# Kernel optimization log

Hardware: AMD Instinct MI355X
Metric: run time of the kernel (lower is better)

Reference implementation:

```python
import jax, jax.numpy as jnp
import numpy as np

MARGIN = 0.3


def setup_inputs() -> dict:
    key = jax.random.key(0)
    k1, k2 = jax.random.split(key)
    inputs = jax.random.normal(k1, (8192, 256), dtype=jnp.float32)
    targets = jax.random.randint(k2, (8192,), 0, 512, dtype=jnp.int64)
    return {"inputs": inputs, "targets": targets}


def reference(inputs, targets):
    # L2-normalize features (normalize_feature=True default)
    x = inputs / (jnp.linalg.norm(inputs, axis=-1, keepdims=True) + 1e-12)
    n = x.shape[0]
    # pairwise euclidean distance [n, n]
    sq = jnp.sum(x * x, axis=1)
    dist = sq[:, None] + sq[None, :] - 2.0 * (x @ x.T)
    dist = jnp.sqrt(jnp.clip(dist, 1e-12, None))
    # positive / negative masks
    same = targets[:, None] == targets[None, :]
    eye = jnp.eye(n, dtype=bool)
    is_same = same & ~eye          # positives, diagonal excluded
    is_diff = ~same                # negatives
    neg_inf = jnp.float32(-jnp.inf)
    pos_inf = jnp.float32(jnp.inf)
    # hard positive: max over positives per row (fallback 0.0 if none)
    dist_ap = jnp.max(jnp.where(is_same, dist, neg_inf), axis=1)
    dist_ap = jnp.where(jnp.any(is_same, axis=1), dist_ap, 0.0)
    # hard negative: min over negatives per row (fallback margin+1 if none)
    dist_an = jnp.min(jnp.where(is_diff, dist, pos_inf), axis=1)
    dist_an = jnp.where(jnp.any(is_diff, axis=1), dist_an, MARGIN + 1.0)
    # MarginRankingLoss with y=1: mean(max(0, -(an - ap) + margin))
    loss = jnp.mean(jnp.maximum(0.0, dist_ap - dist_an + MARGIN))
    return loss
```

## Files before the change

### kernel.cpp

```cpp
#include <hip/hip_runtime.h>
#include <hip/hip_bf16.h>

#define NROWS  8192
#define DIM    256
#define NCLASS 512
#define MARGIN 0.3f

using bf16x8 = __attribute__((ext_vector_type(8))) short;
using f32x4  = __attribute__((ext_vector_type(4))) float;

__device__ inline ushort f2bf(float f) {
    __hip_bfloat16 h = __float2bfloat16(f);
    return *reinterpret_cast<ushort*>(&h);
}
__device__ inline float bf2f(ushort u) {
    return __uint_as_float(((unsigned)u) << 16);
}
__device__ inline unsigned f2ord(float f) {
    unsigned b = __float_as_uint(f);
    return (b & 0x80000000u) ? ~b : (b | 0x80000000u);
}
__device__ inline float ord2f(unsigned u) {
    return __uint_as_float((u & 0x80000000u) ? (u & 0x7FFFFFFFu) : ~u);
}
__device__ inline void ld16_g2l(const void* g, void* l) {
    __builtin_amdgcn_global_load_lds(
        (const __attribute__((address_space(1))) unsigned int*)g,
        (__attribute__((address_space(3))) unsigned int*)l, 16, 0, 0);
}

#define XBS_OFF 0u
#define SQS_OFF 4194304u
#define TGT_OFF 4227072u
#define PMX_OFF 4259840u
#define NMN_OFF 4292608u
#define BIN_OFF 4325376u
#define ACC_OFF 4327424u
#define TIK_OFF 4327432u

__global__ __launch_bounds__(512) void hist_scan_kernel(
    const int* __restrict__ tgt, int* __restrict__ bincur,
    double* __restrict__ accd, unsigned* __restrict__ ticket)
{
    __shared__ int h[NCLASS];
    int tid = threadIdx.x;
    h[tid] = 0;
    if (tid == 0) { *accd = 0.0; *ticket = 0u; }
    __syncthreads();
    for (int k = 0; k < NROWS / NCLASS; ++k)
        atomicAdd(&h[tgt[tid + k * NCLASS]], 1);
    __syncthreads();
    int cnt = h[tid];
    for (int ofs = 1; ofs < NCLASS; ofs <<= 1) {
        int v = (tid >= ofs) ? h[tid - ofs] : 0;
        __syncthreads();
        h[tid] += v;
        __syncthreads();
    }
    bincur[tid] = h[tid] - cnt;
}

__global__ __launch_bounds__(256) void norm_scatter_kernel(
    const float* __restrict__ in, const int* __restrict__ tgt,
    int* __restrict__ bincur, ushort* __restrict__ xbs,
    float* __restrict__ sqs, int* __restrict__ tgts,
    unsigned* __restrict__ pmax, unsigned* __restrict__ nmin)
{
    int row  = blockIdx.x * 4 + (threadIdx.x >> 6);
    int lane = threadIdx.x & 63;
    float4 v = ((const float4*)(in + (size_t)row * DIM))[lane];
    float ss = v.x * v.x + v.y * v.y + v.z * v.z + v.w * v.w;
#pragma unroll
    for (int m = 1; m < 64; m <<= 1) ss += __shfl_xor(ss, m, 64);
    float inv = 1.0f / (sqrtf(ss) + 1e-12f);

    ushort4 st;
    st.x = f2bf(v.x * inv); st.y = f2bf(v.y * inv);
    st.z = f2bf(v.z * inv); st.w = f2bf(v.w * inv);

    int t = 0, dst = 0;
    if (lane == 0) { t = tgt[row]; dst = atomicAdd(&bincur[t], 1); }
    dst = __shfl(dst, 0); t = __shfl(t, 0);

    ((ushort4*)(xbs + (size_t)dst * DIM))[lane] = st;

    float a0 = bf2f(st.x), a1 = bf2f(st.y), a2 = bf2f(st.z), a3 = bf2f(st.w);
    float s2 = a0 * a0 + a1 * a1 + a2 * a2 + a3 * a3;
#pragma unroll
    for (int m = 1; m < 64; m <<= 1) s2 += __shfl_xor(s2, m, 64);
    if (lane == 0) {
        sqs[dst]  = s2;
        tgts[dst] = t;
        pmax[dst] = 0x007FFFFFu;
        nmin[dst] = 0xFF800000u;
    }
}

__global__ __launch_bounds__(256, 2) void gram_kernel(
    const ushort* __restrict__ xbs, const float* __restrict__ sqs,
    const int* __restrict__ tgts, unsigned* __restrict__ pmax,
    unsigned* __restrict__ nmin)
{
    __shared__ struct {
        char  buf[2][16384];
        float sqc[512];
        int   tgc[512];
        int   tga[256];
    } sm;

    const int wave = threadIdx.x >> 6;
    const int lane = threadIdx.x & 63;
    const int l15  = lane & 15;
    const int quad = lane >> 4;
    const int mbase = blockIdx.x * 256 + wave * 64;
    const int nbase = blockIdx.y * 512;

    {
        int c = threadIdx.x * 2;
        sm.sqc[c]     = sqs[nbase + c];
        sm.sqc[c + 1] = sqs[nbase + c + 1];
        sm.tgc[c]     = tgts[nbase + c];
        sm.tgc[c + 1] = tgts[nbase + c + 1];
        sm.tga[threadIdx.x] = tgts[blockIdx.x * 256 + threadIdx.x];
    }

    bf16x8 afrag[4][8];
#pragma unroll
    for (int a = 0; a < 4; ++a) {
        const ushort* arow = xbs + (size_t)(mbase + a * 16 + l15) * DIM + quad * 8;
#pragma unroll
        for (int kk = 0; kk < 8; ++kk)
            afrag[a][kk] = *(const bf16x8*)(arow + kk * 32);
    }
    const int rlo = tgts[mbase];
    const int rhi = tgts[mbase + 63];

    const int colh = lane >> 5, c31 = lane & 31;
    int offs[4];
#pragma unroll
    for (int j = 0; j < 4; ++j)
        offs[j] = colh * 512 + ((c31 ^ ((2 * j + colh) & 7)) << 4);

    const char* xbs_b = (const char*)xbs;

    {
        const char* gbase = xbs_b + (size_t)nbase * 512;
#pragma unroll
        for (int j = 0; j < 4; ++j) {
            int i = wave * 4 + j;
            ld16_g2l(gbase + i * 1024 + offs[j], sm.buf[0] + i * 1024);
        }
    }
    __syncthreads();

    float pm[16], nm[16];
#pragma unroll
    for (int j = 0; j < 16; ++j) { pm[j] = -__builtin_inff(); nm[j] = __builtin_inff(); }

#pragma unroll 2
    for (int s = 0; s < 16; ++s) {
        if (s < 15) {
            const char* gbase = xbs_b + (size_t)(nbase + (s + 1) * 32) * 512;
            char* lbase = sm.buf[(s + 1) & 1];
#pragma unroll
            for (int j = 0; j < 4; ++j) {
                int i = wave * 4 + j;
                ld16_g2l(gbase + i * 1024 + offs[j], lbase + i * 1024);
            }
        }
        const char* bufc = sm.buf[s & 1];
#pragma unroll
        for (int u = 0; u < 2; ++u) {
            const int t16 = s * 32 + u * 16;
            bf16x8 bfrag[8];
#pragma unroll
            for (int kk = 0; kk < 8; ++kk)
                bfrag[kk] = *(const bf16x8*)(bufc + u * 8192 + l15 * 512 +
                                             (((quad + 4 * kk) ^ (l15 & 7)) << 4));
            f32x4 acc4[4];
#pragma unroll
            for (int a = 0; a < 4; ++a) {
                f32x4 acc = {0.f, 0.f, 0.f, 0.f};
#pragma unroll
                for (int kk = 0; kk < 8; ++kk)
                    acc = __builtin_amdgcn_mfma_f32_16x16x32_bf16(afrag[a][kk], bfrag[kk], acc, 0, 0, 0);
                acc4[a] = acc;
            }
            const float sqc = sm.sqc[t16 + l15];
            const int clo = sm.tgc[t16], chi = sm.tgc[t16 + 15];
            if (rlo <= chi && clo <= rhi) {
                const int tc = sm.tgc[t16 + l15];
#pragma unroll
                for (int a = 0; a < 4; ++a)
#pragma unroll
                    for (int i = 0; i < 4; ++i) {
                        const float v = fmaf(acc4[a][i], -2.0f, sqc);
                        const bool same = (sm.tga[wave * 64 + a * 16 + quad * 4 + i] == tc);
                        pm[a * 4 + i] = fmaxf(pm[a * 4 + i], same ? v : -__builtin_inff());
                        nm[a * 4 + i] = fminf(nm[a * 4 + i], same ? __builtin_inff() : v);
                    }
            } else {
#pragma unroll
                for (int a = 0; a < 4; ++a)
#pragma unroll
                    for (int i = 0; i < 4; ++i)
                        nm[a * 4 + i] = fminf(nm[a * 4 + i], fmaf(acc4[a][i], -2.0f, sqc));
            }
        }
        __syncthreads();
    }

#pragma unroll
    for (int m = 1; m < 16; m <<= 1) {
#pragma unroll
        for (int j = 0; j < 16; ++j) {
            pm[j] = fmaxf(pm[j], __shfl_xor(pm[j], m, 64));
            nm[j] = fminf(nm[j], __shfl_xor(nm[j], m, 64));
        }
    }
    if (l15 == 0) {
#pragma unroll
        for (int a = 0; a < 4; ++a)
#pragma unroll
            for (int i = 0; i < 4; ++i) {
                int r = mbase + a * 16 + quad * 4 + i;
                atomicMax(&pmax[r], f2ord(pm[a * 4 + i]));
                atomicMin(&nmin[r], f2ord(nm[a * 4 + i]));
            }
    }
}

__global__ __launch_bounds__(256) void finalize_kernel(
    const unsigned* __restrict__ pmax, const unsigned* __restrict__ nmin,
    const float* __restrict__ sqs, double* __restrict__ accd,
    unsigned* __restrict__ ticket, float* __restrict__ out)
{
    int r = blockIdx.x * 256 + threadIdx.x;
    float pe = ord2f(pmax[r]);
    float ne = ord2f(nmin[r]);
    float ap = sqrtf(fmaxf(sqs[r] + pe, 0.0f));
    float an = (ne > 1e30f) ? (MARGIN + 1.0f) : sqrtf(fmaxf(sqs[r] + ne, 0.0f));
    float h  = fmaxf(ap - an + MARGIN, 0.0f);
    double s = (double)h;
#pragma unroll
    for (int m = 1; m < 64; m <<= 1) s += __shfl_xor(s, m, 64);
    __shared__ double sh[4];
    if ((threadIdx.x & 63) == 0) sh[threadIdx.x >> 6] = s;
    __syncthreads();
    if (threadIdx.x == 0) {
        double b = sh[0] + sh[1] + sh[2] + sh[3];
        atomicAdd(accd, b);
        __threadfence();
        unsigned old = atomicAdd(ticket, 1u);
        if (old == gridDim.x - 1) {
            double total = atomicAdd(accd, 0.0);
            out[0] = (float)(total / (double)NROWS);
        }
    }
}

extern "C" void kernel_launch(void* const* d_in, const int* in_sizes, int n_in,
                              void* d_out, int out_size, void* d_ws, size_t ws_size,
                              hipStream_t stream) {
    const float* in  = (const float*)d_in[0];
    const int*   tgt = (const int*)d_in[1];
    float*       out = (float*)d_out;

    char* ws = (char*)d_ws;
    ushort*   xbs    = (ushort*)(ws + XBS_OFF);
    float*    sqs    = (float*)(ws + SQS_OFF);
    int*      tgts   = (int*)(ws + TGT_OFF);
    unsigned* pmax   = (unsigned*)(ws + PMX_OFF);
    unsigned* nmin   = (unsigned*)(ws + NMN_OFF);
    int*      bincur = (int*)(ws + BIN_OFF);
    double*   accd   = (double*)(ws + ACC_OFF);
    unsigned* ticket = (unsigned*)(ws + TIK_OFF);

    hist_scan_kernel<<<1, 512, 0, stream>>>(tgt, bincur, accd, ticket);
    norm_scatter_kernel<<<NROWS / 4, 256, 0, stream>>>(in, tgt, bincur, xbs, sqs, tgts, pmax, nmin);
    gram_kernel<<<dim3(32, 16), 256, 0, stream>>>(xbs, sqs, tgts, pmax, nmin);
    finalize_kernel<<<32, 256, 0, stream>>>(pmax, nmin, sqs, accd, ticket, out);
}
```

Measured before the change: 113.9 us.

## Fuse all stages into one persistent kernel with grid barriers and permutation indirection

Replaces the four launches (histogram/scan, normalize+scatter, gram, finalize) with a single 512-block kernel that uses software grid barriers between phases and a last-block ticket for the final reduction. Rows are no longer physically scattered into class order; instead block 0 builds a permutation, and the gram phase gathers rows through it. The intent is to remove launch gaps and the extra scatter writes. In exchange it adds a serial single-block phase (scan plus an 8192-row perm build), spin-wait barriers that assume all 512 blocks are co-resident, indirect gathered loads, and a memset launch.

```diff
diff --git a/kernel.cpp b/kernel.cpp
--- a/kernel.cpp
+++ b/kernel.cpp
@@ -4,7 +4,11 @@
 #define NROWS  8192
 #define DIM    256
 #define NCLASS 512
+#define NBLK   512
 #define MARGIN 0.3f
+
+#define ORD_NEGINF 0x007FFFFFu
+#define ORD_POSINF 0xFF800000u
 
 using bf16x8 = __attribute__((ext_vector_type(8))) short;
 using f32x4  = __attribute__((ext_vector_type(4))) float;
@@ -29,126 +33,146 @@
         (__attribute__((address_space(3))) unsigned int*)l, 16, 0, 0);
 }
 
-#define XBS_OFF 0u
-#define SQS_OFF 4194304u
-#define TGT_OFF 4227072u
-#define PMX_OFF 4259840u
-#define NMN_OFF 4292608u
-#define BIN_OFF 4325376u
-#define ACC_OFF 4327424u
-#define TIK_OFF 4327432u
-
-__global__ __launch_bounds__(512) void hist_scan_kernel(
-    const int* __restrict__ tgt, int* __restrict__ bincur,
-    double* __restrict__ accd, unsigned* __restrict__ ticket)
+#define XB_OFF   0u
+#define SQU_OFF  4194304u
+#define PRM_OFF  4227072u
+#define SQS_OFF  4259840u
+#define TGS_OFF  4292608u
+#define PMX_OFF  4325376u
+#define NMN_OFF  4358144u
+#define META_OFF 4390912u
+
+struct SM {
+    char  buf[2][16384];
+    float sqc[512];
+    int   tgc[512];
+    int   prm[512];
+    int   tga[256];
+};
+
+__device__ inline void grid_barrier(unsigned* cnt) {
+    __syncthreads();
+    if (threadIdx.x == 0) {
+        __threadfence();
+        atomicAdd(cnt, 1u);
+        while (atomicAdd(cnt, 0u) < NBLK) __builtin_amdgcn_s_sleep(2);
+        __threadfence();
+    }
+    __syncthreads();
+}
+
+__global__ __launch_bounds__(256, 2) void fused_kernel(
+    const float* __restrict__ in, const int* __restrict__ tgt,
+    ushort* __restrict__ xb, float* __restrict__ squ,
+    int* __restrict__ perm, float* __restrict__ sqs, int* __restrict__ tgts,
+    unsigned* __restrict__ pmax, unsigned* __restrict__ nmin,
+    int* __restrict__ bins, unsigned* __restrict__ bar1,
+    unsigned* __restrict__ bar2, unsigned* __restrict__ ticket,
+    float* __restrict__ out)
 {
-    __shared__ int h[NCLASS];
-    int tid = threadIdx.x;
-    h[tid] = 0;
-    if (tid == 0) { *accd = 0.0; *ticket = 0u; }
-    __syncthreads();
-    for (int k = 0; k < NROWS / NCLASS; ++k)
-        atomicAdd(&h[tgt[tid + k * NCLASS]], 1);
-    __syncthreads();
-    int cnt = h[tid];
-    for (int ofs = 1; ofs < NCLASS; ofs <<= 1) {
-        int v = (tid >= ofs) ? h[tid - ofs] : 0;
-        __syncthreads();
-        h[tid] += v;
-        __syncthreads();
-    }
-    bincur[tid] = h[tid] - cnt;
-}
-
-__global__ __launch_bounds__(256) void norm_scatter_kernel(
-    const float* __restrict__ in, const int* __restrict__ tgt,
-    int* __restrict__ bincur, ushort* __restrict__ xbs,
-    float* __restrict__ sqs, int* __restrict__ tgts,
-    unsigned* __restrict__ pmax, unsigned* __restrict__ nmin)
-{
-    int row  = blockIdx.x * 4 + (threadIdx.x >> 6);
-    int lane = threadIdx.x & 63;
-    float4 v = ((const float4*)(in + (size_t)row * DIM))[lane];
-    float ss = v.x * v.x + v.y * v.y + v.z * v.z + v.w * v.w;
-#pragma unroll
-    for (int m = 1; m < 64; m <<= 1) ss += __shfl_xor(ss, m, 64);
-    float inv = 1.0f / (sqrtf(ss) + 1e-12f);
-
-    ushort4 st;
-    st.x = f2bf(v.x * inv); st.y = f2bf(v.y * inv);
-    st.z = f2bf(v.z * inv); st.w = f2bf(v.w * inv);
-
-    int t = 0, dst = 0;
-    if (lane == 0) { t = tgt[row]; dst = atomicAdd(&bincur[t], 1); }
-    dst = __shfl(dst, 0); t = __shfl(t, 0);
-
-    ((ushort4*)(xbs + (size_t)dst * DIM))[lane] = st;
-
-    float a0 = bf2f(st.x), a1 = bf2f(st.y), a2 = bf2f(st.z), a3 = bf2f(st.w);
-    float s2 = a0 * a0 + a1 * a1 + a2 * a2 + a3 * a3;
-#pragma unroll
-    for (int m = 1; m < 64; m <<= 1) s2 += __shfl_xor(s2, m, 64);
-    if (lane == 0) {
-        sqs[dst]  = s2;
-        tgts[dst] = t;
-        pmax[dst] = 0x007FFFFFu;
-        nmin[dst] = 0xFF800000u;
-    }
-}
-
-__global__ __launch_bounds__(256, 2) void gram_kernel(
-    const ushort* __restrict__ xbs, const float* __restrict__ sqs,
-    const int* __restrict__ tgts, unsigned* __restrict__ pmax,
-    unsigned* __restrict__ nmin)
-{
-    __shared__ struct {
-        char  buf[2][16384];
-        float sqc[512];
-        int   tgc[512];
-        int   tga[256];
-    } sm;
-
-    const int wave = threadIdx.x >> 6;
-    const int lane = threadIdx.x & 63;
+    __shared__ SM sm;
+    __shared__ unsigned lastflag;
+    const int b    = blockIdx.x;
+    const int tid  = threadIdx.x;
+    const int wave = tid >> 6;
+    const int lane = tid & 63;
     const int l15  = lane & 15;
     const int quad = lane >> 4;
-    const int mbase = blockIdx.x * 256 + wave * 64;
-    const int nbase = blockIdx.y * 512;
+
+#pragma unroll
+    for (int i = 0; i < 4; ++i) {
+        int row = b * 16 + wave * 4 + i;
+        float4 v = ((const float4*)(in + (size_t)row * DIM))[lane];
+        float ss = v.x * v.x + v.y * v.y + v.z * v.z + v.w * v.w;
+#pragma unroll
+        for (int m = 1; m < 64; m <<= 1) ss += __shfl_xor(ss, m, 64);
+        float inv = 1.0f / (sqrtf(ss) + 1e-12f);
+        ushort4 st;
+        st.x = f2bf(v.x * inv); st.y = f2bf(v.y * inv);
+        st.z = f2bf(v.z * inv); st.w = f2bf(v.w * inv);
+        ((ushort4*)(xb + (size_t)row * DIM))[lane] = st;
+        float a0 = bf2f(st.x), a1 = bf2f(st.y), a2 = bf2f(st.z), a3 = bf2f(st.w);
+        float s2 = a0 * a0 + a1 * a1 + a2 * a2 + a3 * a3;
+#pragma unroll
+        for (int m = 1; m < 64; m <<= 1) s2 += __shfl_xor(s2, m, 64);
+        if (lane == 0) {
+            squ[row]  = s2;
+            pmax[row] = ORD_NEGINF;
+            nmin[row] = ORD_POSINF;
+            atomicAdd(&bins[tgt[row]], 1);
+        }
+    }
+    grid_barrier(bar1);
+
+    if (b == 0) {
+        int* sc  = (int*)sm.buf[0];
+        int* cur = sc + NCLASS;
+        const int c0 = tid, c1 = tid + 256;
+        sc[c0] = atomicAdd(&bins[c0], 0);
+        sc[c1] = atomicAdd(&bins[c1], 0);
+        __syncthreads();
+        int n0 = sc[c0], n1 = sc[c1];
+        for (int ofs = 1; ofs < NCLASS; ofs <<= 1) {
+            int v0 = (c0 >= ofs) ? sc[c0 - ofs] : 0;
+            int v1 = (c1 >= ofs) ? sc[c1 - ofs] : 0;
+            __syncthreads();
+            sc[c0] += v0; sc[c1] += v1;
+            __syncthreads();
+        }
+        cur[c0] = sc[c0] - n0;
+        cur[c1] = sc[c1] - n1;
+        __syncthreads();
+        for (int it = 0; it < NROWS / 256; ++it) {
+            int r = it * 256 + tid;
+            int c = tgt[r];
+            int slot = atomicAdd(&cur[c], 1);
+            perm[slot] = r;
+            sqs[slot]  = squ[r];
+            tgts[slot] = c;
+        }
+    }
+    grid_barrier(bar2);
+
+    const int bx = b >> 4;
+    const int by = b & 15;
+    const int mbase = bx * 256 + wave * 64;
+    const int nbase = by * 512;
 
     {
-        int c = threadIdx.x * 2;
+        int c = tid * 2;
         sm.sqc[c]     = sqs[nbase + c];
         sm.sqc[c + 1] = sqs[nbase + c + 1];
         sm.tgc[c]     = tgts[nbase + c];
         sm.tgc[c + 1] = tgts[nbase + c + 1];
-        sm.tga[threadIdx.x] = tgts[blockIdx.x * 256 + threadIdx.x];
-    }
+        sm.prm[c]     = perm[nbase + c];
+        sm.prm[c + 1] = perm[nbase + c + 1];
+        sm.tga[tid]   = tgts[bx * 256 + tid];
+    }
+    __syncthreads();
 
     bf16x8 afrag[4][8];
 #pragma unroll
     for (int a = 0; a < 4; ++a) {
-        const ushort* arow = xbs + (size_t)(mbase + a * 16 + l15) * DIM + quad * 8;
+        int grow = perm[mbase + a * 16 + l15];
+        const ushort* arow = xb + (size_t)grow * DIM + quad * 8;
 #pragma unroll
         for (int kk = 0; kk < 8; ++kk)
             afrag[a][kk] = *(const bf16x8*)(arow + kk * 32);
     }
-    const int rlo = tgts[mbase];
-    const int rhi = tgts[mbase + 63];
+    const int rlo = sm.tga[wave * 64];
+    const int rhi = sm.tga[wave * 64 + 63];
 
     const int colh = lane >> 5, c31 = lane & 31;
-    int offs[4];
-#pragma unroll
-    for (int j = 0; j < 4; ++j)
-        offs[j] = colh * 512 + ((c31 ^ ((2 * j + colh) & 7)) << 4);
-
-    const char* xbs_b = (const char*)xbs;
+    const char* xb_b = (const char*)xb;
 
     {
-        const char* gbase = xbs_b + (size_t)nbase * 512;
 #pragma unroll
         for (int j = 0; j < 4; ++j) {
             int i = wave * 4 + j;
-            ld16_g2l(gbase + i * 1024 + offs[j], sm.buf[0] + i * 1024);
+            int col = 2 * i + colh;
+            int prow = sm.prm[col];
+            ld16_g2l(xb_b + (size_t)prow * 512 + ((c31 ^ (col & 7)) << 4),
+                     sm.buf[0] + i * 1024);
         }
     }
     __syncthreads();
@@ -160,12 +184,14 @@
 #pragma unroll 2
     for (int s = 0; s < 16; ++s) {
         if (s < 15) {
-            const char* gbase = xbs_b + (size_t)(nbase + (s + 1) * 32) * 512;
             char* lbase = sm.buf[(s + 1) & 1];
 #pragma unroll
             for (int j = 0; j < 4; ++j) {
                 int i = wave * 4 + j;
-                ld16_g2l(gbase + i * 1024 + offs[j], lbase + i * 1024);
+                int col = 2 * i + colh;
+                int prow = sm.prm[(s + 1) * 32 + col];
+                ld16_g2l(xb_b + (size_t)prow * 512 + ((c31 ^ (col & 7)) << 4),
+                         lbase + i * 1024);
             }
         }
         const char* bufc = sm.buf[s & 1];
@@ -228,34 +254,31 @@
                 atomicMin(&nmin[r], f2ord(nm[a * 4 + i]));
             }
     }
-}
-
-__global__ __launch_bounds__(256) void finalize_kernel(
-    const unsigned* __restrict__ pmax, const unsigned* __restrict__ nmin,
-    const float* __restrict__ sqs, double* __restrict__ accd,
-    unsigned* __restrict__ ticket, float* __restrict__ out)
-{
-    int r = blockIdx.x * 256 + threadIdx.x;
-    float pe = ord2f(pmax[r]);
-    float ne = ord2f(nmin[r]);
-    float ap = sqrtf(fmaxf(sqs[r] + pe, 0.0f));
-    float an = (ne > 1e30f) ? (MARGIN + 1.0f) : sqrtf(fmaxf(sqs[r] + ne, 0.0f));
-    float h  = fmaxf(ap - an + MARGIN, 0.0f);
-    double s = (double)h;
-#pragma unroll
-    for (int m = 1; m < 64; m <<= 1) s += __shfl_xor(s, m, 64);
-    __shared__ double sh[4];
-    if ((threadIdx.x & 63) == 0) sh[threadIdx.x >> 6] = s;
-    __syncthreads();
-    if (threadIdx.x == 0) {
-        double b = sh[0] + sh[1] + sh[2] + sh[3];
-        atomicAdd(accd, b);
+
+    __syncthreads();
+    if (tid == 0) {
         __threadfence();
-        unsigned old = atomicAdd(ticket, 1u);
-        if (old == gridDim.x - 1) {
-            double total = atomicAdd(accd, 0.0);
-            out[0] = (float)(total / (double)NROWS);
-        }
+        unsigned arrived = atomicAdd(ticket, 1u) + 1;
+        lastflag = (arrived == NBLK) ? 1u : 0u;
+    }
+    __syncthreads();
+    if (lastflag) {
+        double s = 0.0;
+        for (int it = 0; it < NROWS / 256; ++it) {
+            int r = it * 256 + tid;
+            float pe = ord2f(atomicMax(&pmax[r], ORD_NEGINF));
+            float ne = ord2f(atomicMin(&nmin[r], ORD_POSINF));
+            float ap = sqrtf(fmaxf(sqs[r] + pe, 0.0f));
+            float an = (ne > 1e30f) ? (MARGIN + 1.0f) : sqrtf(fmaxf(sqs[r] + ne, 0.0f));
+            float h  = fmaxf(ap - an + MARGIN, 0.0f);
+            s += (double)h;
+        }
+#pragma unroll
+        for (int m = 1; m < 64; m <<= 1) s += __shfl_xor(s, m, 64);
+        double* shd = (double*)sm.buf[0];
+        if (lane == 0) shd[wave] = s;
+        __syncthreads();
+        if (tid == 0) out[0] = (float)((shd[0] + shd[1] + shd[2] + shd[3]) / (double)NROWS);
     }
 }
 
@@ -267,17 +290,19 @@
     float*       out = (float*)d_out;
 
     char* ws = (char*)d_ws;
-    ushort*   xbs    = (ushort*)(ws + XBS_OFF);
+    ushort*   xb     = (ushort*)(ws + XB_OFF);
+    float*    squ    = (float*)(ws + SQU_OFF);
+    int*      perm   = (int*)(ws + PRM_OFF);
     float*    sqs    = (float*)(ws + SQS_OFF);
-    int*      tgts   = (int*)(ws + TGT_OFF);
+    int*      tgts   = (int*)(ws + TGS_OFF);
     unsigned* pmax   = (unsigned*)(ws + PMX_OFF);
     unsigned* nmin   = (unsigned*)(ws + NMN_OFF);
-    int*      bincur = (int*)(ws + BIN_OFF);
-    double*   accd   = (double*)(ws + ACC_OFF);
-    unsigned* ticket = (unsigned*)(ws + TIK_OFF);
-
-    hist_scan_kernel<<<1, 512, 0, stream>>>(tgt, bincur, accd, ticket);
-    norm_scatter_kernel<<<NROWS / 4, 256, 0, stream>>>(in, tgt, bincur, xbs, sqs, tgts, pmax, nmin);
-    gram_kernel<<<dim3(32, 16), 256, 0, stream>>>(xbs, sqs, tgts, pmax, nmin);
-    finalize_kernel<<<32, 256, 0, stream>>>(pmax, nmin, sqs, accd, ticket, out);
-}
+    int*      bins   = (int*)(ws + META_OFF);
+    unsigned* bar1   = (unsigned*)(ws + META_OFF + 2048);
+    unsigned* bar2   = (unsigned*)(ws + META_OFF + 2052);
+    unsigned* ticket = (unsigned*)(ws + META_OFF + 2056);
+
+    hipMemsetAsync(ws + META_OFF, 0, 4096, stream);
+    fused_kernel<<<NBLK, 256, 0, stream>>>(in, tgt, xb, squ, perm, sqs, tgts,
+                                           pmax, nmin, bins, bar1, bar2, ticket, out);
+}
```

Result: slower. 217.9 us (+91.3%).

## Store B tiles in fragment-major LDS layout with 64-column stages

Applied to the files above, without the earlier changes.

Reorganizes the LDS staging of B (column) rows so each wave loads 16 rows directly into an MFMA-fragment-ordered layout, so each lane reads contiguous 16-byte chunks at lane*16 with no XOR swizzle. Stage size doubles from 32 to 64 columns (LDS buffers grow to 2x32KB) and the stage count halves, reducing barriers and prefetch overhead. The larger shared memory footprint may reduce occupancy under launch_bounds(256,2). The global loads now read 64-byte strided pieces per row, which may coalesce less well.

```diff
diff --git a/kernel.cpp b/kernel.cpp
--- a/kernel.cpp
+++ b/kernel.cpp
@@ -102,7 +102,7 @@
     unsigned* __restrict__ nmin)
 {
     __shared__ struct {
-        char  buf[2][16384];
+        char  buf[2][32768];
         float sqc[512];
         int   tgc[512];
         int   tga[256];
@@ -135,21 +135,15 @@
     const int rlo = tgts[mbase];
     const int rhi = tgts[mbase + 63];
 
-    const int colh = lane >> 5, c31 = lane & 31;
-    int offs[4];
-#pragma unroll
-    for (int j = 0; j < 4; ++j)
-        offs[j] = colh * 512 + ((c31 ^ ((2 * j + colh) & 7)) << 4);
-
+    const int loff = l15 * 512 + quad * 16;
     const char* xbs_b = (const char*)xbs;
 
     {
-        const char* gbase = xbs_b + (size_t)nbase * 512;
-#pragma unroll
-        for (int j = 0; j < 4; ++j) {
-            int i = wave * 4 + j;
-            ld16_g2l(gbase + i * 1024 + offs[j], sm.buf[0] + i * 1024);
-        }
+        const char* gsrc = xbs_b + (size_t)(nbase + wave * 16) * 512 + loff;
+        char* ldst = sm.buf[0] + wave * 8192;
+#pragma unroll
+        for (int kk = 0; kk < 8; ++kk)
+            ld16_g2l(gsrc + kk * 64, ldst + kk * 1024);
     }
     __syncthreads();
 
@@ -158,25 +152,22 @@
     for (int j = 0; j < 16; ++j) { pm[j] = -__builtin_inff(); nm[j] = __builtin_inff(); }
 
 #pragma unroll 2
-    for (int s = 0; s < 16; ++s) {
-        if (s < 15) {
-            const char* gbase = xbs_b + (size_t)(nbase + (s + 1) * 32) * 512;
-            char* lbase = sm.buf[(s + 1) & 1];
-#pragma unroll
-            for (int j = 0; j < 4; ++j) {
-                int i = wave * 4 + j;
-                ld16_g2l(gbase + i * 1024 + offs[j], lbase + i * 1024);
-            }
-        }
-        const char* bufc = sm.buf[s & 1];
-#pragma unroll
-        for (int u = 0; u < 2; ++u) {
-            const int t16 = s * 32 + u * 16;
+    for (int s = 0; s < 8; ++s) {
+        if (s < 7) {
+            const char* gsrc = xbs_b + (size_t)(nbase + (s + 1) * 64 + wave * 16) * 512 + loff;
+            char* ldst = sm.buf[(s + 1) & 1] + wave * 8192;
+#pragma unroll
+            for (int kk = 0; kk < 8; ++kk)
+                ld16_g2l(gsrc + kk * 64, ldst + kk * 1024);
+        }
+        const char* bb = sm.buf[s & 1] + lane * 16;
+#pragma unroll
+        for (int u = 0; u < 4; ++u) {
+            const int t16 = s * 64 + u * 16;
             bf16x8 bfrag[8];
 #pragma unroll
             for (int kk = 0; kk < 8; ++kk)
-                bfrag[kk] = *(const bf16x8*)(bufc + u * 8192 + l15 * 512 +
-                                             (((quad + 4 * kk) ^ (l15 & 7)) << 4));
+                bfrag[kk] = *(const bf16x8*)(bb + u * 8192 + kk * 1024);
             f32x4 acc4[4];
 #pragma unroll
             for (int a = 0; a < 4; ++a) {
```

After: 115.8 us. About the same (+1.7%).
